# Kernel optimization log

Hardware: AMD Instinct MI355X
Metric: run time of the kernel (lower is better)

The kernel has to match this reference:

```python
import jax, jax.numpy as jnp
import numpy as np
import math

B, N, L, D = 8, 128, 30, 256


def setup_inputs() -> dict:
    key = jax.random.key(0)
    ks = jax.random.split(key, 8)
    return {
        "f_b": jax.random.normal(ks[0], (B, N, D), jnp.float32),
        "f_w": jax.random.normal(ks[1], (B, L, D), jnp.float32),
        "f_s": jax.random.normal(ks[2], (B, D), jnp.float32),
        "f_m": jax.random.normal(ks[3], (B, N, N, D), jnp.float32),
        "query_mask": jnp.ones((B, L), jnp.float32),
        "length_mask": jnp.ones((B, N), jnp.float32),
        "Wq": jax.random.normal(ks[4], (D, D), jnp.float32) / math.sqrt(D),
        "bq": jax.random.normal(ks[5], (D,), jnp.float32) * 0.02,
        "Wk": jax.random.normal(ks[6], (D, D), jnp.float32) / math.sqrt(D),
        "bk": jax.random.normal(ks[7], (D,), jnp.float32) * 0.02,
    }


def reference(f_b, f_w, f_s, f_m, query_mask, length_mask, Wq, bq, Wk, bk):
    d = f_b.shape[-1]
    scale = 1.0 / math.sqrt(d)
    NEG = -1e9

    # --- Attention(f_b over f_w) ---
    q = f_b @ Wq.T + bq                                   # [B,N,D]
    k = f_w @ Wk.T + bk                                   # [B,L,D]
    aw = jnp.einsum('bnd,bld->bnl', q, k) * scale         # [B,N,L]
    qm = query_mask[:, None, :]                           # [B,1,L]
    aw = jnp.where(qm == 0, NEG, aw * qm)
    aw = jax.nn.softmax(aw, axis=-1)
    f_baq = jnp.einsum('bnl,bld->bnd', aw, f_w)           # [B,N,D]

    fb_mask = length_mask[:, :, None]                     # [B,N,1]
    f_baq = f_baq * fb_mask
    f_bq = f_b * (f_baq + f_s[:, None, :])                # [B,N,D]

    # --- self-attention over boundary features ---
    A = jnp.einsum('bnd,bmd->bnm', f_bq, f_bq) * scale    # [B,N,N]
    lm = length_mask[:, None, :]                          # [B,1,N]
    A = jnp.where(lm == 0, NEG, A * lm)
    A = jax.nn.softmax(A, axis=-1) * fb_mask              # [B,N,N]
    f_bb = jnp.einsum('bnm,bmd->bnd', A, f_b) * fb_mask

    # --- gated aggregation over the 2D moment map ---
    g_m = jax.nn.sigmoid(f_m * f_s[:, None, None, :])     # [B,N,N,D]
    f_bm = jnp.einsum('bnm,bnmd->bnd', A, g_m * f_m)      # [B,N,D]

    return f_bb + f_b + f_bm
```

## Files before the change

### kernel.cpp

```cpp
#include <hip/hip_runtime.h>
#include <math.h>

#define B_ 8
#define N_ 128
#define L_ 30
#define D_ 256
#define NEGV -1000000000.0f
#define SCALE 0.0625f

__global__ __launch_bounds__(256) void w2prep(const float* __restrict__ Wk,
    const float* __restrict__ Wq, const float* __restrict__ bq,
    const float* __restrict__ bk, float* __restrict__ W2,
    float* __restrict__ wbq, float* __restrict__ bbc0) {
  int blk = blockIdx.x;
  int t = threadIdx.x, wave = t >> 6, lane = t & 63;
  __shared__ float col[D_];
  __shared__ float wsum[4];

  if (blk < 256) {
    int d = blk;
    col[t] = Wk[(size_t)t * D_ + d];
    __syncthreads();
    float a0 = 0.f, a1 = 0.f, a2 = 0.f, a3 = 0.f;
#pragma unroll 4
    for (int c4 = 0; c4 < 64; ++c4) {
      float4 kv = ((const float4*)col)[c4];
      a0 += kv.x * Wq[(size_t)(4*c4+0) * D_ + t];
      a1 += kv.y * Wq[(size_t)(4*c4+1) * D_ + t];
      a2 += kv.z * Wq[(size_t)(4*c4+2) * D_ + t];
      a3 += kv.w * Wq[(size_t)(4*c4+3) * D_ + t];
    }
    W2[(size_t)d * D_ + t] = (a0 + a1) + (a2 + a3);
    float p = bq[t] * col[t];
#pragma unroll
    for (int off = 32; off >= 1; off >>= 1) p += __shfl_xor(p, off);
    if (lane == 0) wsum[wave] = p;
    __syncthreads();
    if (t == 0) wbq[d] = wsum[0] + wsum[1] + wsum[2] + wsum[3];
  } else {
    float a0 = 0.f, a1 = 0.f, a2 = 0.f, a3 = 0.f;
#pragma unroll 4
    for (int c = 0; c < D_; c += 4) {
      a0 += bk[c + 0] * Wq[(size_t)(c + 0) * D_ + t];
      a1 += bk[c + 1] * Wq[(size_t)(c + 1) * D_ + t];
      a2 += bk[c + 2] * Wq[(size_t)(c + 2) * D_ + t];
      a3 += bk[c + 3] * Wq[(size_t)(c + 3) * D_ + t];
    }
    bbc0[t] = (a0 + a1) + (a2 + a3);
    float p = bq[t] * bk[t];
#pragma unroll
    for (int off = 32; off >= 1; off >>= 1) p += __shfl_xor(p, off);
    if (lane == 0) wsum[wave] = p;
    __syncthreads();
    if (t == 0) bbc0[D_] = wsum[0] + wsum[1] + wsum[2] + wsum[3];
  }
}

__global__ __launch_bounds__(256) void k2row(const float* __restrict__ f_w,
    const float* __restrict__ W2, const float* __restrict__ wbq,
    const float* __restrict__ bbc0, float* __restrict__ k2f,
    float* __restrict__ sv) {
  int l = blockIdx.x;
  int t = threadIdx.x, wave = t >> 6, lane = t & 63;
  __shared__ float fw[D_];
  __shared__ float wsum[4];
  fw[t] = f_w[(size_t)l * D_ + t];
  __syncthreads();
  float a0 = 0.f, a1 = 0.f, a2 = 0.f, a3 = 0.f;
#pragma unroll 4
  for (int d4 = 0; d4 < 64; ++d4) {
    float4 fv = ((const float4*)fw)[d4];
    a0 += fv.x * W2[(size_t)(4*d4+0) * D_ + t];
    a1 += fv.y * W2[(size_t)(4*d4+1) * D_ + t];
    a2 += fv.z * W2[(size_t)(4*d4+2) * D_ + t];
    a3 += fv.w * W2[(size_t)(4*d4+3) * D_ + t];
  }
  k2f[(size_t)l * D_ + t] = (a0 + a1) + (a2 + a3) + bbc0[t];
  float p = fw[t] * wbq[t];
#pragma unroll
  for (int off = 32; off >= 1; off >>= 1) p += __shfl_xor(p, off);
  if (lane == 0) wsum[wave] = p;
  __syncthreads();
  if (t == 0) sv[l] = wsum[0] + wsum[1] + wsum[2] + wsum[3] + bbc0[D_];
}

__global__ __launch_bounds__(256) void aw_fbq(const float* __restrict__ f_b,
    const float* __restrict__ f_w, const float* __restrict__ f_s,
    const float* __restrict__ qmask, const float* __restrict__ lmask,
    const float* __restrict__ k2f, const float* __restrict__ sv,
    float* __restrict__ fbq) {
  int blk = blockIdx.x;
  int b = blk >> 5, n0 = (blk & 31) * 4;
  int t = threadIdx.x;

  __shared__ float k2l[L_][260];
  __shared__ float fbl[4][260];
  __shared__ float pdot[120][2];
  __shared__ float awl[4][32];
  __shared__ float slds[32];

  for (int r = 0; r < 4; ++r)
    fbl[r][t] = f_b[(size_t)(b * N_ + n0 + r) * D_ + t];
  for (int l = 0; l < L_; ++l)
    k2l[l][t] = k2f[(size_t)(b * L_ + l) * D_ + t];
  if (t < L_) slds[t] = sv[b * L_ + t];
  __syncthreads();

  if (t < 240) {
    int p = t % 120, half = t / 120;
    int r = p / 30, l = p % 30;
    const float4* fr = (const float4*)(fbl[r] + half * 128);
    const float4* kr = (const float4*)(k2l[l] + half * 128);
    float ac[4] = {0.f, 0.f, 0.f, 0.f};
#pragma unroll
    for (int j = 0; j < 32; ++j) {
      float4 fv = fr[j], kv = kr[j];
      ac[j & 3] += fv.x*kv.x + fv.y*kv.y + fv.z*kv.z + fv.w*kv.w;
    }
    pdot[p][half] = (ac[0] + ac[1]) + (ac[2] + ac[3]);
  }
  __syncthreads();

  if (t < 120) {
    int r = t / 30, l = t % 30;
    float acc = pdot[t][0] + pdot[t][1];
    float aw = (acc + slds[l]) * SCALE;
    float qm = qmask[b * L_ + l];
    awl[r][l] = (qm == 0.f) ? NEGV : aw * qm;
  }
  __syncthreads();

  if (t < 4) {
    float mx = -1e30f;
    for (int l = 0; l < L_; ++l) mx = fmaxf(mx, awl[t][l]);
    float s = 0.f;
    for (int l = 0; l < L_; ++l) { float e = __expf(awl[t][l] - mx); awl[t][l] = e; s += e; }
    float inv = 1.f / s;
    for (int l = 0; l < L_; ++l) awl[t][l] *= inv;
  }
  __syncthreads();

  for (int l = 0; l < L_; ++l)
    k2l[l][t] = f_w[(size_t)(b * L_ + l) * D_ + t];
  __syncthreads();

  float fsd = f_s[b * D_ + t];
  for (int r = 0; r < 4; ++r) {
    float f0 = 0.f, f1 = 0.f;
#pragma unroll
    for (int l = 0; l < L_; l += 2) {
      f0 += awl[r][l] * k2l[l][t];
      f1 += awl[r][l + 1] * k2l[l + 1][t];
    }
    float lm = lmask[b * N_ + n0 + r];
    fbq[(size_t)(b * N_ + n0 + r) * D_ + t] = fbl[r][t] * ((f0 + f1) * lm + fsd);
  }
}

__global__ __launch_bounds__(256) void fused_stream(const float* __restrict__ f_b,
    const float* __restrict__ f_m, const float* __restrict__ f_s,
    const float* __restrict__ lmask, const float* __restrict__ fbq,
    float* __restrict__ out) {
  int bn = blockIdx.x, b = bn >> 7, n = bn & 127;
  int t = threadIdx.x, w = t >> 6, lane = t & 63;

  __shared__ float part[4][32][65];
  __shared__ float a_lds[N_];
  __shared__ float sm[8];
  __shared__ float4 red[3][64];

  const float4* fmb = (const float4*)(f_m + (size_t)bn * N_ * D_);
  const float4* fbb = (const float4*)(f_b + (size_t)b * N_ * D_);
  int m0 = w * 32;

  float4 pA[8], pB[8];
#pragma unroll
  for (int i = 0; i < 8; ++i) pA[i] = fmb[(size_t)(m0 + i) * 64 + lane];
  __builtin_amdgcn_sched_barrier(0);

  float4 qv = ((const float4*)(fbq + (size_t)bn * D_))[lane];
#pragma unroll 8
  for (int i = 0; i < 32; ++i) {
    float4 v = ((const float4*)(fbq + (size_t)(b * N_ + m0 + i) * D_))[lane];
    part[w][i][lane] = v.x*qv.x + v.y*qv.y + v.z*qv.z + v.w*qv.w;
  }
  __syncthreads();
  float s = 0.f;
#pragma unroll
  for (int j = 0; j < 32; ++j)
    s += part[w][lane & 31][(lane >> 5) * 32 + j];
  s += __shfl_xor(s, 32);
  if (lane < 32) a_lds[m0 + (lane & 31)] = s;
  __syncthreads();

  float lmn = lmask[b * N_ + n];
  float e = 0.f;
  if (t < N_) {
    float lm = lmask[b * N_ + t];
    float v = (lm == 0.f) ? NEGV : a_lds[t] * SCALE * lm;
    float mx = v;
#pragma unroll
    for (int off = 32; off >= 1; off >>= 1) mx = fmaxf(mx, __shfl_xor(mx, off));
    if (lane == 0) sm[w] = mx;
  }
  __syncthreads();
  if (t < N_) {
    float lm = lmask[b * N_ + t];
    float v = (lm == 0.f) ? NEGV : a_lds[t] * SCALE * lm;
    float gmax = fmaxf(sm[0], sm[1]);
    e = __expf(v - gmax);
    float ss = e;
#pragma unroll
    for (int off = 32; off >= 1; off >>= 1) ss += __shfl_xor(ss, off);
    if (lane == 0) sm[4 + w] = ss;
  }
  __syncthreads();
  if (t < N_) {
    float tot = sm[4] + sm[5];
    a_lds[t] = e * (lmn / tot);
  }
  __syncthreads();

  float4 fs4 = ((const float4*)(f_s + (size_t)b * D_))[lane];
  const float CLOG = -1.44269504088896f;
  float4 cs;
  cs.x = fs4.x * CLOG; cs.y = fs4.y * CLOG;
  cs.z = fs4.z * CLOG; cs.w = fs4.w * CLOG;
  float4 acc = make_float4(0.f, 0.f, 0.f, 0.f);

  auto compute8 = [&](float4 (&P)[8], int mbase) {
#pragma unroll
    for (int i = 0; i < 8; ++i) {
      int m = mbase + i;
      float a = a_lds[m];
      float4 fb4 = fbb[(size_t)m * 64 + lane];
      float4 fm4 = P[i];
      float gx = __builtin_amdgcn_rcpf(1.f + __builtin_amdgcn_exp2f(fm4.x * cs.x));
      float gy = __builtin_amdgcn_rcpf(1.f + __builtin_amdgcn_exp2f(fm4.y * cs.y));
      float gz = __builtin_amdgcn_rcpf(1.f + __builtin_amdgcn_exp2f(fm4.z * cs.z));
      float gw = __builtin_amdgcn_rcpf(1.f + __builtin_amdgcn_exp2f(fm4.w * cs.w));
      acc.x += a * (lmn * fb4.x + gx * fm4.x);
      acc.y += a * (lmn * fb4.y + gy * fm4.y);
      acc.z += a * (lmn * fb4.z + gz * fm4.z);
      acc.w += a * (lmn * fb4.w + gw * fm4.w);
    }
  };

#pragma unroll
  for (int i = 0; i < 8; ++i) pB[i] = fmb[(size_t)(m0 + 8 + i) * 64 + lane];
  compute8(pA, m0);
#pragma unroll
  for (int i = 0; i < 8; ++i) pA[i] = fmb[(size_t)(m0 + 16 + i) * 64 + lane];
  compute8(pB, m0 + 8);
#pragma unroll
  for (int i = 0; i < 8; ++i) pB[i] = fmb[(size_t)(m0 + 24 + i) * 64 + lane];
  compute8(pA, m0 + 16);
  compute8(pB, m0 + 24);

  if (w > 0) red[w - 1][lane] = acc;
  __syncthreads();
  if (w == 0) {
#pragma unroll
    for (int j = 0; j < 3; ++j) {
      float4 r4 = red[j][lane];
      acc.x += r4.x; acc.y += r4.y; acc.z += r4.z; acc.w += r4.w;
    }
    float4 fbn = fbb[(size_t)n * 64 + lane];
    float4 o;
    o.x = fbn.x + acc.x;
    o.y = fbn.y + acc.y;
    o.z = fbn.z + acc.z;
    o.w = fbn.w + acc.w;
    ((float4*)out)[(size_t)bn * 64 + lane] = o;
  }
}

extern "C" void kernel_launch(void* const* d_in, const int* in_sizes, int n_in,
                              void* d_out, int out_size, void* d_ws, size_t ws_size,
                              hipStream_t stream) {
  const float* f_b   = (const float*)d_in[0];
  const float* f_w   = (const float*)d_in[1];
  const float* f_s   = (const float*)d_in[2];
  const float* f_m   = (const float*)d_in[3];
  const float* qmask = (const float*)d_in[4];
  const float* lmask = (const float*)d_in[5];
  const float* Wq    = (const float*)d_in[6];
  const float* bq    = (const float*)d_in[7];
  const float* Wk    = (const float*)d_in[8];
  const float* bk    = (const float*)d_in[9];
  float* out = (float*)d_out;

  float* ws   = (float*)d_ws;
  float* W2   = ws;
  float* wbq  = ws + 65536;
  float* bbc0 = ws + 66048;
  float* k2f  = ws + 131072;
  float* sv   = ws + 196608;
  float* fbq  = ws + 262144;

  hipLaunchKernelGGL(w2prep, dim3(257), dim3(256), 0, stream,
                     Wk, Wq, bq, bk, W2, wbq, bbc0);
  hipLaunchKernelGGL(k2row, dim3(B_ * L_), dim3(256), 0, stream,
                     f_w, W2, wbq, bbc0, k2f, sv);
  hipLaunchKernelGGL(aw_fbq, dim3(256), dim3(256), 0, stream,
                     f_b, f_w, f_s, qmask, lmask, k2f, sv, fbq);
  hipLaunchKernelGGL(fused_stream, dim3(B_ * N_), dim3(256), 0, stream,
                     f_b, f_m, f_s, lmask, fbq, out);
}
```

Baseline: 62.35 us.

## Compute key projection per row instead of precomputing Wk^T·Wq product matrix

Removes the w2prep kernel, which built the combined W2 = Wk^T Wq matrix plus bias terms, and merges it with k2row into one kernel. Each of the B*L blocks now computes k = Wk·f_w + bk with a wave-level matvec and LDS partial sums, then projects k through Wq. This drops one kernel launch and the dependent 256x256x256 weight product, at the cost of an extra per-row matvec against Wk.

```diff
diff --git a/kernel.cpp b/kernel.cpp
--- a/kernel.cpp
+++ b/kernel.cpp
@@ -8,80 +8,52 @@
 #define NEGV -1000000000.0f
 #define SCALE 0.0625f
 
-__global__ __launch_bounds__(256) void w2prep(const float* __restrict__ Wk,
+__global__ __launch_bounds__(256) void kk2(const float* __restrict__ f_w,
+    const float* __restrict__ Wk, const float* __restrict__ bk,
     const float* __restrict__ Wq, const float* __restrict__ bq,
-    const float* __restrict__ bk, float* __restrict__ W2,
-    float* __restrict__ wbq, float* __restrict__ bbc0) {
-  int blk = blockIdx.x;
-  int t = threadIdx.x, wave = t >> 6, lane = t & 63;
-  __shared__ float col[D_];
-  __shared__ float wsum[4];
-
-  if (blk < 256) {
-    int d = blk;
-    col[t] = Wk[(size_t)t * D_ + d];
-    __syncthreads();
-    float a0 = 0.f, a1 = 0.f, a2 = 0.f, a3 = 0.f;
-#pragma unroll 4
-    for (int c4 = 0; c4 < 64; ++c4) {
-      float4 kv = ((const float4*)col)[c4];
-      a0 += kv.x * Wq[(size_t)(4*c4+0) * D_ + t];
-      a1 += kv.y * Wq[(size_t)(4*c4+1) * D_ + t];
-      a2 += kv.z * Wq[(size_t)(4*c4+2) * D_ + t];
-      a3 += kv.w * Wq[(size_t)(4*c4+3) * D_ + t];
-    }
-    W2[(size_t)d * D_ + t] = (a0 + a1) + (a2 + a3);
-    float p = bq[t] * col[t];
-#pragma unroll
-    for (int off = 32; off >= 1; off >>= 1) p += __shfl_xor(p, off);
-    if (lane == 0) wsum[wave] = p;
-    __syncthreads();
-    if (t == 0) wbq[d] = wsum[0] + wsum[1] + wsum[2] + wsum[3];
-  } else {
-    float a0 = 0.f, a1 = 0.f, a2 = 0.f, a3 = 0.f;
-#pragma unroll 4
-    for (int c = 0; c < D_; c += 4) {
-      a0 += bk[c + 0] * Wq[(size_t)(c + 0) * D_ + t];
-      a1 += bk[c + 1] * Wq[(size_t)(c + 1) * D_ + t];
-      a2 += bk[c + 2] * Wq[(size_t)(c + 2) * D_ + t];
-      a3 += bk[c + 3] * Wq[(size_t)(c + 3) * D_ + t];
-    }
-    bbc0[t] = (a0 + a1) + (a2 + a3);
-    float p = bq[t] * bk[t];
-#pragma unroll
-    for (int off = 32; off >= 1; off >>= 1) p += __shfl_xor(p, off);
-    if (lane == 0) wsum[wave] = p;
-    __syncthreads();
-    if (t == 0) bbc0[D_] = wsum[0] + wsum[1] + wsum[2] + wsum[3];
-  }
-}
-
-__global__ __launch_bounds__(256) void k2row(const float* __restrict__ f_w,
-    const float* __restrict__ W2, const float* __restrict__ wbq,
-    const float* __restrict__ bbc0, float* __restrict__ k2f,
-    float* __restrict__ sv) {
+    float* __restrict__ k2f, float* __restrict__ sv) {
   int l = blockIdx.x;
   int t = threadIdx.x, wave = t >> 6, lane = t & 63;
-  __shared__ float fw[D_];
+  __shared__ float part[4][16][65];
+  __shared__ float kl[D_];
   __shared__ float wsum[4];
-  fw[t] = f_w[(size_t)l * D_ + t];
-  __syncthreads();
+
+  float4 x4 = ((const float4*)(f_w + (size_t)l * D_))[lane];
+
+  for (int g = 0; g < 4; ++g) {
+    int dbase = wave * 64 + g * 16;
+#pragma unroll
+    for (int i = 0; i < 16; ++i) {
+      float4 w4 = ((const float4*)(Wk + (size_t)(dbase + i) * D_))[lane];
+      part[wave][i][lane] = w4.x*x4.x + w4.y*x4.y + w4.z*x4.z + w4.w*x4.w;
+    }
+    float s = 0.f;
+#pragma unroll
+    for (int j = 0; j < 16; ++j)
+      s += part[wave][lane & 15][(lane >> 4) * 16 + j];
+    s += __shfl_xor(s, 16);
+    s += __shfl_xor(s, 32);
+    if (lane < 16) kl[dbase + lane] = s + bk[dbase + lane];
+  }
+  __syncthreads();
+
   float a0 = 0.f, a1 = 0.f, a2 = 0.f, a3 = 0.f;
 #pragma unroll 4
   for (int d4 = 0; d4 < 64; ++d4) {
-    float4 fv = ((const float4*)fw)[d4];
-    a0 += fv.x * W2[(size_t)(4*d4+0) * D_ + t];
-    a1 += fv.y * W2[(size_t)(4*d4+1) * D_ + t];
-    a2 += fv.z * W2[(size_t)(4*d4+2) * D_ + t];
-    a3 += fv.w * W2[(size_t)(4*d4+3) * D_ + t];
-  }
-  k2f[(size_t)l * D_ + t] = (a0 + a1) + (a2 + a3) + bbc0[t];
-  float p = fw[t] * wbq[t];
+    float4 kv = ((const float4*)kl)[d4];
+    a0 += kv.x * Wq[(size_t)(4*d4+0) * D_ + t];
+    a1 += kv.y * Wq[(size_t)(4*d4+1) * D_ + t];
+    a2 += kv.z * Wq[(size_t)(4*d4+2) * D_ + t];
+    a3 += kv.w * Wq[(size_t)(4*d4+3) * D_ + t];
+  }
+  k2f[(size_t)l * D_ + t] = (a0 + a1) + (a2 + a3);
+
+  float p = bq[t] * kl[t];
 #pragma unroll
   for (int off = 32; off >= 1; off >>= 1) p += __shfl_xor(p, off);
   if (lane == 0) wsum[wave] = p;
   __syncthreads();
-  if (t == 0) sv[l] = wsum[0] + wsum[1] + wsum[2] + wsum[3] + bbc0[D_];
+  if (t == 0) sv[l] = wsum[0] + wsum[1] + wsum[2] + wsum[3];
 }
 
 __global__ __launch_bounds__(256) void aw_fbq(const float* __restrict__ f_b,
@@ -290,18 +262,13 @@
   const float* bk    = (const float*)d_in[9];
   float* out = (float*)d_out;
 
-  float* ws   = (float*)d_ws;
-  float* W2   = ws;
-  float* wbq  = ws + 65536;
-  float* bbc0 = ws + 66048;
-  float* k2f  = ws + 131072;
-  float* sv   = ws + 196608;
-  float* fbq  = ws + 262144;
-
-  hipLaunchKernelGGL(w2prep, dim3(257), dim3(256), 0, stream,
-                     Wk, Wq, bq, bk, W2, wbq, bbc0);
-  hipLaunchKernelGGL(k2row, dim3(B_ * L_), dim3(256), 0, stream,
-                     f_w, W2, wbq, bbc0, k2f, sv);
+  float* ws  = (float*)d_ws;
+  float* k2f = ws;
+  float* sv  = ws + 65536;
+  float* fbq = ws + 131072;
+
+  hipLaunchKernelGGL(kk2, dim3(B_ * L_), dim3(256), 0, stream,
+                     f_w, Wk, bk, Wq, bq, k2f, sv);
   hipLaunchKernelGGL(aw_fbq, dim3(256), dim3(256), 0, stream,
                      f_b, f_w, f_s, qmask, lmask, k2f, sv, fbq);
   hipLaunchKernelGGL(fused_stream, dim3(B_ * N_), dim3(256), 0, stream,
```

Result: faster. 57.89 us (-7.2%).
